# Kernel tuning notes

Hardware: AMD Instinct MI355X
Metric: run time of the kernel (lower is better)

The kernel has to match this reference:

```python
import jax, jax.numpy as jnp
import numpy as np

BATCH = 8
MAX_SEQ = 2048
HEAD_NUM = 16  # num_attention_heads_per_partition


def setup_inputs() -> dict:
    key = jax.random.key(0)
    k1, k2 = jax.random.split(key)
    attention_mask = jax.random.uniform(k1, (BATCH, 1, MAX_SEQ, MAX_SEQ), dtype=jnp.float16)
    # ragged per-sequence lengths in [1, MAX_SEQ]; concrete (shape params, not traced)
    seq_lengths = np.asarray(jax.random.randint(k2, (BATCH,), 1, MAX_SEQ + 1), dtype=np.int32)
    return {"attention_mask": attention_mask, "seq_lengths": seq_lengths}


def reference(attention_mask, seq_lengths):
    # Pack the top-left s_i x s_i block of each batch's mask, replicated across
    # HEAD_NUM heads, into one flat fp16 buffer; then threshold > 0.5 -> bool.
    mask = attention_mask.astype(jnp.float16)
    lens = [int(s) for s in np.asarray(seq_lengths)]  # static shape params
    pieces = []
    for i, s in enumerate(lens):
        block = mask[i, 0, :s, :s]                        # [s, s]
        rep = jnp.broadcast_to(block, (HEAD_NUM, s, s))   # replicate per head
        pieces.append(rep.reshape(-1))                    # [HEAD_NUM*s*s]
    packed = jnp.concatenate(pieces)                      # [sum_i HEAD_NUM*s_i^2]
    return packed > jnp.float16(0.5)
```

## Files before the change

### kernel.cpp

```cpp
#include <hip/hip_runtime.h>

#define THREADS 256
#define WAVES_PB 4
#define ITERS 4
#define MAX_BLOCKS 8192

__global__ void setup_offsets_kernel(const int* __restrict__ seq,
                                     unsigned int* __restrict__ ws) {
    if (threadIdx.x == 0 && blockIdx.x == 0) {
        unsigned int o16 = 0, cs = 0;
        ws[0] = 0u; ws[9] = 0u;
        for (int b = 0; b < 8; ++b) {
            unsigned int s  = (unsigned int)seq[b];
            unsigned int s2 = s * s;
            o16 += 16u * s2;
            cs  += (s2 + 255u) >> 8;
            ws[1 + b]  = o16;
            ws[10 + b] = cs;
            ws[18 + b] = s;
            ws[26 + b] = s2;
            ((float*)ws)[34 + b] = 1.0f / (float)s;
        }
    }
}

__global__ void __launch_bounds__(THREADS)
unpad_mask_kernel(const float* __restrict__ mask,
                  const unsigned int* __restrict__ ws,
                  int* __restrict__ out) {
    __shared__ unsigned int off16[9];
    __shared__ unsigned int csum[9];
    __shared__ unsigned int slen[8];
    __shared__ unsigned int ssq[8];
    __shared__ float        sinv[8];

    int tx = threadIdx.x;
    if (tx < 9) { off16[tx] = ws[tx]; csum[tx] = ws[9 + tx]; }
    if (tx < 8) {
        slen[tx] = ws[18 + tx];
        ssq[tx]  = ws[26 + tx];
        sinv[tx] = ((const float*)ws)[34 + tx];
    }
    __syncthreads();

    unsigned int nchunks = csum[8];
    unsigned int wave_id = blockIdx.x * WAVES_PB + ((unsigned int)tx >> 6);
    unsigned int lane    = (unsigned int)tx & 63u;

#pragma unroll 1
    for (int it = 0; it < ITERS; ++it) {
        unsigned int chunk = wave_id * ITERS + (unsigned int)it;
        if (chunk >= nchunks) break;

        unsigned int b = 0;
#pragma unroll
        for (int j = 1; j < 8; ++j) b += (chunk >= csum[j]) ? 1u : 0u;

        unsigned int s    = slen[b];
        unsigned int s2   = ssq[b];
        float        inv  = sinv[b];
        unsigned int p0   = (chunk - csum[b]) << 8;
        unsigned int base = off16[b];
        const float* mb   = mask + ((size_t)b << 22);

        if (s2 - p0 >= 256u) {
            unsigned int q   = p0 + (lane << 2);
            unsigned int row = (unsigned int)((float)q * inv);
            int col = (int)q - (int)(row * s);
            if (col < 0)            { row -= 1u; col += (int)s; }
            else if (col >= (int)s) { row += 1u; col -= (int)s; }

            unsigned int r0 = row;  int c0 = col;
            float v0 = mb[(size_t)r0 * 2048u + (unsigned int)c0];
            c0++; if (c0 == (int)s) { c0 = 0; r0++; }
            float v1 = mb[(size_t)r0 * 2048u + (unsigned int)c0];
            c0++; if (c0 == (int)s) { c0 = 0; r0++; }
            float v2 = mb[(size_t)r0 * 2048u + (unsigned int)c0];
            c0++; if (c0 == (int)s) { c0 = 0; r0++; }
            float v3 = mb[(size_t)r0 * 2048u + (unsigned int)c0];

            int o0 = (v0 > 0.5f) ? 1 : 0;
            int o1 = (v1 > 0.5f) ? 1 : 0;
            int o2 = (v2 > 0.5f) ? 1 : 0;
            int o3 = (v3 > 0.5f) ? 1 : 0;
            int4 o4  = make_int4(o0, o1, o2, o3);
            int2 o2a = make_int2(o0, o1);
            int2 o2b = make_int2(o2, o3);

            if ((s & 1u) == 0u) {
                unsigned int off = base + q;
#pragma unroll
                for (int h = 0; h < 16; ++h) {
                    *(int4*)(out + off) = o4;
                    off += s2;
                }
            } else {
                unsigned int off = base + q;
#pragma unroll
                for (int h = 0; h < 16; ++h) {
                    if ((h & 3) == 0) {
                        *(int4*)(out + off) = o4;
                    } else if ((h & 3) == 2) {
                        *(int2*)(out + off)     = o2a;
                        *(int2*)(out + off + 2) = o2b;
                    } else {
                        out[off]     = o0;
                        out[off + 1] = o1;
                        out[off + 2] = o2;
                        out[off + 3] = o3;
                    }
                    off += s2;
                }
            }
        } else {
#pragma unroll
            for (int j = 0; j < 4; ++j) {
                unsigned int p = p0 + (lane << 2) + (unsigned int)j;
                if (p >= s2) continue;
                unsigned int row = (unsigned int)((float)p * inv);
                int col = (int)p - (int)(row * s);
                if (col < 0)            { row -= 1u; col += (int)s; }
                else if (col >= (int)s) { row += 1u; col -= (int)s; }
                float v = mb[(size_t)row * 2048u + (unsigned int)col];
                int o = (v > 0.5f) ? 1 : 0;
                unsigned int off = base + p;
#pragma unroll
                for (int h = 0; h < 16; ++h) {
                    out[off] = o;
                    off += s2;
                }
            }
        }
    }
}

extern "C" void kernel_launch(void* const* d_in, const int* in_sizes, int n_in,
                              void* d_out, int out_size, void* d_ws, size_t ws_size,
                              hipStream_t stream) {
    const float*  mask = (const float*)d_in[0];
    const int*    seq  = (const int*)d_in[1];
    unsigned int* ws   = (unsigned int*)d_ws;
    int*          out  = (int*)d_out;

    setup_offsets_kernel<<<1, 64, 0, stream>>>(seq, ws);
    unpad_mask_kernel<<<MAX_BLOCKS, THREADS, 0, stream>>>(mask, ws, out);
}
```

Baseline: 727.2 us.

## Tile over output elements so every wave writes aligned int4 stores

The kernel now splits work into 1024-element tiles of the packed output instead of 256-position tiles of the source block. Each wave writes contiguous aligned int4 stores, rather than replicating each loaded value across 16 heads with strided, possibly misaligned stores. The fixed four-iterations-per-wave scheme is replaced by a grid-stride loop. The aim is fully coalesced, vectorized writes. In exchange, each mask element is re-read once per head, which adds reads served mostly from cache, plus extra division and modulo arithmetic.

After: 718.4 us. No clear change (-1.2%).

```diff
diff --git a/kernel.cpp b/kernel.cpp
--- a/kernel.cpp
+++ b/kernel.cpp
@@ -2,24 +2,25 @@
 
 #define THREADS 256
 #define WAVES_PB 4
-#define ITERS 4
 #define MAX_BLOCKS 8192
 
 __global__ void setup_offsets_kernel(const int* __restrict__ seq,
                                      unsigned int* __restrict__ ws) {
     if (threadIdx.x == 0 && blockIdx.x == 0) {
-        unsigned int o16 = 0, cs = 0;
+        unsigned int oE = 0, cs = 0;
         ws[0] = 0u; ws[9] = 0u;
         for (int b = 0; b < 8; ++b) {
-            unsigned int s  = (unsigned int)seq[b];
-            unsigned int s2 = s * s;
-            o16 += 16u * s2;
-            cs  += (s2 + 255u) >> 8;
-            ws[1 + b]  = o16;
+            unsigned int s    = (unsigned int)seq[b];
+            unsigned int s2   = s * s;
+            unsigned int nout = s2 << 4;
+            oE += nout;
+            cs += (nout + 1023u) >> 10;
+            ws[1 + b]  = oE;
             ws[10 + b] = cs;
             ws[18 + b] = s;
             ws[26 + b] = s2;
             ((float*)ws)[34 + b] = 1.0f / (float)s;
+            ((float*)ws)[42 + b] = 1.0f / (float)s2;
         }
     }
 }
@@ -28,30 +29,30 @@
 unpad_mask_kernel(const float* __restrict__ mask,
                   const unsigned int* __restrict__ ws,
                   int* __restrict__ out) {
-    __shared__ unsigned int off16[9];
+    __shared__ unsigned int offE[9];
     __shared__ unsigned int csum[9];
     __shared__ unsigned int slen[8];
     __shared__ unsigned int ssq[8];
     __shared__ float        sinv[8];
+    __shared__ float        sinv2[8];
 
     int tx = threadIdx.x;
-    if (tx < 9) { off16[tx] = ws[tx]; csum[tx] = ws[9 + tx]; }
+    if (tx < 9) { offE[tx] = ws[tx]; csum[tx] = ws[9 + tx]; }
     if (tx < 8) {
-        slen[tx] = ws[18 + tx];
-        ssq[tx]  = ws[26 + tx];
-        sinv[tx] = ((const float*)ws)[34 + tx];
+        slen[tx]  = ws[18 + tx];
+        ssq[tx]   = ws[26 + tx];
+        sinv[tx]  = ((const float*)ws)[34 + tx];
+        sinv2[tx] = ((const float*)ws)[42 + tx];
     }
     __syncthreads();
 
-    unsigned int nchunks = csum[8];
-    unsigned int wave_id = blockIdx.x * WAVES_PB + ((unsigned int)tx >> 6);
-    unsigned int lane    = (unsigned int)tx & 63u;
+    unsigned int nchunks     = csum[8];
+    unsigned int total_waves = gridDim.x * WAVES_PB;
+    unsigned int wave_id     = blockIdx.x * WAVES_PB + ((unsigned int)tx >> 6);
+    unsigned int lane        = (unsigned int)tx & 63u;
 
 #pragma unroll 1
-    for (int it = 0; it < ITERS; ++it) {
-        unsigned int chunk = wave_id * ITERS + (unsigned int)it;
-        if (chunk >= nchunks) break;
-
+    for (unsigned int chunk = wave_id; chunk < nchunks; chunk += total_waves) {
         unsigned int b = 0;
 #pragma unroll
         for (int j = 1; j < 8; ++j) b += (chunk >= csum[j]) ? 1u : 0u;
@@ -59,75 +60,65 @@
         unsigned int s    = slen[b];
         unsigned int s2   = ssq[b];
         float        inv  = sinv[b];
-        unsigned int p0   = (chunk - csum[b]) << 8;
-        unsigned int base = off16[b];
+        float        inv2 = sinv2[b];
+        unsigned int tb   = (chunk - csum[b]) << 10;
+        unsigned int nout = s2 << 4;
+        unsigned int gbase = offE[b] + tb;
         const float* mb   = mask + ((size_t)b << 22);
 
-        if (s2 - p0 >= 256u) {
-            unsigned int q   = p0 + (lane << 2);
-            unsigned int row = (unsigned int)((float)q * inv);
-            int col = (int)q - (int)(row * s);
-            if (col < 0)            { row -= 1u; col += (int)s; }
-            else if (col >= (int)s) { row += 1u; col -= (int)s; }
+        if (s2 >= 1024u && tb + 1024u <= nout) {
+            unsigned int h  = (unsigned int)((float)tb * inv2);
+            int pbi = (int)tb - (int)(h * s2);
+            while (pbi < 0)          pbi += (int)s2;
+            while (pbi >= (int)s2)   pbi -= (int)s2;
+            unsigned int pb = (unsigned int)pbi;
 
-            unsigned int r0 = row;  int c0 = col;
-            float v0 = mb[(size_t)r0 * 2048u + (unsigned int)c0];
-            c0++; if (c0 == (int)s) { c0 = 0; r0++; }
-            float v1 = mb[(size_t)r0 * 2048u + (unsigned int)c0];
-            c0++; if (c0 == (int)s) { c0 = 0; r0++; }
-            float v2 = mb[(size_t)r0 * 2048u + (unsigned int)c0];
-            c0++; if (c0 == (int)s) { c0 = 0; r0++; }
-            float v3 = mb[(size_t)r0 * 2048u + (unsigned int)c0];
+#pragma unroll
+            for (int sub = 0; sub < 4; ++sub) {
+                unsigned int p = pb + ((unsigned int)sub << 8) + (lane << 2);
+                if (p >= s2) p -= s2;
 
-            int o0 = (v0 > 0.5f) ? 1 : 0;
-            int o1 = (v1 > 0.5f) ? 1 : 0;
-            int o2 = (v2 > 0.5f) ? 1 : 0;
-            int o3 = (v3 > 0.5f) ? 1 : 0;
-            int4 o4  = make_int4(o0, o1, o2, o3);
-            int2 o2a = make_int2(o0, o1);
-            int2 o2b = make_int2(o2, o3);
-
-            if ((s & 1u) == 0u) {
-                unsigned int off = base + q;
-#pragma unroll
-                for (int h = 0; h < 16; ++h) {
-                    *(int4*)(out + off) = o4;
-                    off += s2;
-                }
-            } else {
-                unsigned int off = base + q;
-#pragma unroll
-                for (int h = 0; h < 16; ++h) {
-                    if ((h & 3) == 0) {
-                        *(int4*)(out + off) = o4;
-                    } else if ((h & 3) == 2) {
-                        *(int2*)(out + off)     = o2a;
-                        *(int2*)(out + off + 2) = o2b;
-                    } else {
-                        out[off]     = o0;
-                        out[off + 1] = o1;
-                        out[off + 2] = o2;
-                        out[off + 3] = o3;
-                    }
-                    off += s2;
-                }
-            }
-        } else {
-#pragma unroll
-            for (int j = 0; j < 4; ++j) {
-                unsigned int p = p0 + (lane << 2) + (unsigned int)j;
-                if (p >= s2) continue;
                 unsigned int row = (unsigned int)((float)p * inv);
                 int col = (int)p - (int)(row * s);
                 if (col < 0)            { row -= 1u; col += (int)s; }
                 else if (col >= (int)s) { row += 1u; col -= (int)s; }
-                float v = mb[(size_t)row * 2048u + (unsigned int)col];
-                int o = (v > 0.5f) ? 1 : 0;
-                unsigned int off = base + p;
+
+                unsigned int r0 = row;  int c0 = col;
+                float v0 = mb[(size_t)r0 * 2048u + (unsigned int)c0];
+                c0++; if (c0 == (int)s) { c0 = 0; r0++; if (r0 == s) r0 = 0u; }
+                float v1 = mb[(size_t)r0 * 2048u + (unsigned int)c0];
+                c0++; if (c0 == (int)s) { c0 = 0; r0++; if (r0 == s) r0 = 0u; }
+                float v2 = mb[(size_t)r0 * 2048u + (unsigned int)c0];
+                c0++; if (c0 == (int)s) { c0 = 0; r0++; if (r0 == s) r0 = 0u; }
+                float v3 = mb[(size_t)r0 * 2048u + (unsigned int)c0];
+
+                int4 o = make_int4((v0 > 0.5f) ? 1 : 0,
+                                   (v1 > 0.5f) ? 1 : 0,
+                                   (v2 > 0.5f) ? 1 : 0,
+                                   (v3 > 0.5f) ? 1 : 0);
+                *(int4*)(out + gbase + ((unsigned int)sub << 8) + (lane << 2)) = o;
+            }
+        } else {
+#pragma unroll 1
+            for (int sub = 0; sub < 4; ++sub) {
 #pragma unroll
-                for (int h = 0; h < 16; ++h) {
-                    out[off] = o;
-                    off += s2;
+                for (int j = 0; j < 4; ++j) {
+                    unsigned int eo = ((unsigned int)sub << 8) + (lane << 2) + (unsigned int)j;
+                    unsigned int e  = tb + eo;
+                    if (e >= nout) continue;
+                    unsigned int h = (unsigned int)((float)e * inv2);
+                    int pi = (int)e - (int)(h * s2);
+                    while (pi < 0)        pi += (int)s2;
+                    while (pi >= (int)s2) pi -= (int)s2;
+                    unsigned int p = (unsigned int)pi;
+
+                    unsigned int row = (unsigned int)((float)p * inv);
+                    int col = (int)p - (int)(row * s);
+                    if (col < 0)            { row -= 1u; col += (int)s; }
+                    else if (col >= (int)s) { row += 1u; col -= (int)s; }
+
+                    float v = mb[(size_t)row * 2048u + (unsigned int)col];
+                    out[gbase + eo] = (v > 0.5f) ? 1 : 0;
                 }
             }
         }
```
